# Performance work log

Hardware: AMD Instinct MI355X
Metric: run time of the kernel (lower is better)

## Reference

```python
import jax, jax.numpy as jnp
import numpy as np

N_NODES = 100000
N_EDGES = 3200000
NFEAT = 256
NHID = 256
NCLASS = 64


def setup_inputs() -> dict:
    key = jax.random.key(0)
    ks = jax.random.split(key, 12)
    x = jax.random.normal(ks[0], (N_NODES, NFEAT), dtype=jnp.float32)
    edge_src = jax.random.randint(ks[1], (N_EDGES,), 0, N_NODES, dtype=jnp.int32)
    edge_dst = jnp.sort(jax.random.randint(ks[2], (N_EDGES,), 0, N_NODES, dtype=jnp.int32))
    edge_w = jax.random.uniform(ks[3], (N_EDGES,), dtype=jnp.float32)
    s1 = 1.0 / np.sqrt(NFEAT)
    s2 = 1.0 / np.sqrt(NHID)
    W1 = jax.random.normal(ks[4], (NFEAT, NHID), dtype=jnp.float32) * s1
    b1 = jnp.zeros((NHID,), dtype=jnp.float32)
    W2 = jax.random.normal(ks[5], (NHID, NHID), dtype=jnp.float32) * s2
    b2 = jnp.zeros((NHID,), dtype=jnp.float32)
    WL1 = jax.random.normal(ks[6], (NHID, NCLASS), dtype=jnp.float32) * s2
    bL1 = jnp.zeros((NCLASS,), dtype=jnp.float32)
    WL2 = jax.random.normal(ks[7], (NHID, NCLASS), dtype=jnp.float32) * s2
    bL2 = jnp.zeros((NCLASS,), dtype=jnp.float32)
    return {"x": x, "edge_src": edge_src, "edge_dst": edge_dst, "edge_w": edge_w,
            "W1": W1, "b1": b1, "W2": W2, "b2": b2,
            "WL1": WL1, "bL1": bL1, "WL2": WL2, "bL2": bL2}


def reference(x, edge_src, edge_dst, edge_w, W1, b1, W2, b2, WL1, bL1, WL2, bL2):
    n = x.shape[0]

    def spmm(h):
        # adj @ h with adj given as (src, dst, w) edge list:
        # out[dst] += w * h[src]
        return jax.ops.segment_sum(edge_w[:, None] * h[edge_src], edge_dst, num_segments=n)

    # GraphConvolution layer 1: support = x @ W; out = adj @ support + b; relu
    # (dropout inactive in eval mode)
    h = jax.nn.relu(spmm(x @ W1) + b1)
    # GraphConvolution layer 2
    h = jax.nn.relu(spmm(h @ W2) + b2)
    # twin dense heads
    logit1 = h @ WL1 + bL1
    logit2 = h @ WL2 + bL2
    return (logit1, logit2)
```

## Files before the change

### kernel.cpp

```cpp
#include <hip/hip_runtime.h>
#include <hip/hip_bf16.h>

typedef __attribute__((ext_vector_type(8))) short short8;
typedef __attribute__((ext_vector_type(4))) float f32x4;
typedef __attribute__((ext_vector_type(2))) float f32x2;

__device__ inline unsigned short f2bf(float f) {
    union { float f; unsigned int u; } x; x.f = f;
    return (unsigned short)((x.u + 0x7fffu + ((x.u >> 16) & 1u)) >> 16);
}

#define ASYNC16(gptr, lptr)                                                      \
    __builtin_amdgcn_global_load_lds(                                            \
        (const __attribute__((address_space(1))) unsigned int*)(gptr),           \
        (__attribute__((address_space(3))) unsigned int*)(lptr), 16, 0, 0)

__device__ __host__ inline int sg(int j) {
    int p = j & 63;
    return (j & ~63) | ((p >> 2) + 16 * (p & 3));
}

__global__ void rowptr_kernel(const int* __restrict__ dst, int* __restrict__ rp,
                              int E, int N) {
    int e = blockIdx.x * blockDim.x + threadIdx.x;
    if (e >= E) return;
    int d1 = dst[e];
    int d0 = (e == 0) ? -1 : dst[e - 1];
    for (int n = d0 + 1; n <= d1; n++) rp[n] = e;
    if (e <= N) {
        int dlast = dst[E - 1];
        if (e > dlast) rp[e] = E;
    }
}

__global__ void x2bf_kernel(const float* __restrict__ x, unsigned short* __restrict__ xb,
                            int n8) {
    int i = blockIdx.x * blockDim.x + threadIdx.x;
    if (i >= n8) return;
    const uint4* p = (const uint4*)(x + (size_t)i * 8);
    uint4 u = p[0], v = p[1];
    uint4 pk;
    pk.x = ((u.x + 0x8000u) >> 16) | ((u.y + 0x8000u) & 0xffff0000u);
    pk.y = ((u.z + 0x8000u) >> 16) | ((u.w + 0x8000u) & 0xffff0000u);
    pk.z = ((v.x + 0x8000u) >> 16) | ((v.y + 0x8000u) & 0xffff0000u);
    pk.w = ((v.z + 0x8000u) >> 16) | ((v.w + 0x8000u) & 0xffff0000u);
    *(uint4*)(xb + (size_t)i * 8) = pk;
}

__global__ void prep_kernel(const float* __restrict__ W1, const float* __restrict__ W2,
                            const float* __restrict__ WL1, const float* __restrict__ WL2,
                            const float* __restrict__ b1, const float* __restrict__ b2,
                            unsigned short* __restrict__ W1t, unsigned short* __restrict__ W2t,
                            unsigned short* __restrict__ WLt,
                            float* __restrict__ b1p, float* __restrict__ b2p) {
    int b = blockIdx.x, k = threadIdx.x;
    if (b < 256) {
        W1t[(size_t)b * 256 + k] = f2bf(W1[(size_t)k * 256 + b]);
    } else if (b < 512) {
        int n = b - 256;
        W2t[(size_t)n * 256 + k] = f2bf(W2[(size_t)sg(k) * 256 + n]);
    } else if (b < 640) {
        int c = b - 512;
        int ks = sg(k);
        float v = (c < 64) ? WL1[(size_t)ks * 64 + c] : WL2[(size_t)ks * 64 + (c - 64)];
        WLt[(size_t)c * 256 + k] = f2bf(v);
    } else if (b == 640) {
        b1p[k] = b1[sg(k)];
    } else {
        b2p[k] = b2[sg(k)];
    }
}

__global__ __launch_bounds__(256) void gemm_f8_kernel(
    const unsigned short* __restrict__ A, const unsigned short* __restrict__ Bt,
    unsigned char* __restrict__ C, int M)
{
    __shared__ __align__(16) unsigned short As[128 * 32];
    __shared__ __align__(16) unsigned short Bs[128 * 32];
    const int t = threadIdx.x;
    const int row0 = blockIdx.y * 128;
    const int col0 = blockIdx.x * 128;
    const int wid = t >> 6, lane = t & 63;
    const int wm = (wid >> 1) * 64, wn = (wid & 1) * 64;
    const int qk = (lane >> 4) * 8, r16 = lane & 15;

    const int c0 = t, c1 = t + 256;
    const int am0 = min(row0 + (c0 >> 2), M - 1);
    const int am1 = min(row0 + (c1 >> 2), M - 1);
    const int ak0 = (c0 & 3) * 8, ak1 = (c1 & 3) * 8;
    const int bm0 = col0 + (c0 >> 2), bm1 = col0 + (c1 >> 2);

    f32x4 acc[4][4];
#pragma unroll
    for (int i = 0; i < 4; i++)
#pragma unroll
        for (int j = 0; j < 4; j++) acc[i][j] = (f32x4){0.f, 0.f, 0.f, 0.f};

    for (int k0 = 0; k0 < 256; k0 += 32) {
        ASYNC16(A + (size_t)am0 * 256 + k0 + ak0, &As[c0 * 8]);
        ASYNC16(A + (size_t)am1 * 256 + k0 + ak1, &As[c1 * 8]);
        ASYNC16(Bt + (size_t)bm0 * 256 + k0 + ak0, &Bs[c0 * 8]);
        ASYNC16(Bt + (size_t)bm1 * 256 + k0 + ak1, &Bs[c1 * 8]);
        __syncthreads();
        short8 av[4], bv[4];
#pragma unroll
        for (int mt = 0; mt < 4; mt++) av[mt] = *(const short8*)(&As[(wm + mt * 16 + r16) * 32 + qk]);
#pragma unroll
        for (int nt = 0; nt < 4; nt++) bv[nt] = *(const short8*)(&Bs[(wn + nt * 16 + r16) * 32 + qk]);
#pragma unroll
        for (int mt = 0; mt < 4; mt++)
#pragma unroll
            for (int nt = 0; nt < 4; nt++)
                acc[mt][nt] = __builtin_amdgcn_mfma_f32_16x16x32_bf16(av[mt], bv[nt], acc[mt][nt], 0, 0, 0);
        __syncthreads();
    }
#pragma unroll
    for (int mt = 0; mt < 4; mt++) {
        const int rowb = row0 + wm + mt * 16 + (lane >> 4) * 4;
#pragma unroll
        for (int r = 0; r < 4; r++) {
            const int row = rowb + r;
            if (row >= M) continue;
            int w = 0;
            w = __builtin_amdgcn_cvt_pk_fp8_f32(acc[mt][0][r], acc[mt][1][r], w, false);
            w = __builtin_amdgcn_cvt_pk_fp8_f32(acc[mt][2][r], acc[mt][3][r], w, true);
            *(unsigned int*)(C + (size_t)row * 256 + col0 + wn + r16 * 4) = (unsigned int)w;
        }
    }
}

__global__ __launch_bounds__(256) void head_kernel(
    const unsigned short* __restrict__ A, const unsigned short* __restrict__ Bt,
    const float* __restrict__ bL1, const float* __restrict__ bL2,
    float* __restrict__ out, int M)
{
    __shared__ __align__(16) unsigned short As[128 * 32];
    __shared__ __align__(16) unsigned short Bs[128 * 32];
    const int t = threadIdx.x;
    const int row0 = blockIdx.x * 128;
    const int wid = t >> 6, lane = t & 63;
    const int wm = (wid >> 1) * 64, wn = (wid & 1) * 64;
    const int qk = (lane >> 4) * 8, r16 = lane & 15;

    const int c0 = t, c1 = t + 256;
    const int am0 = min(row0 + (c0 >> 2), M - 1);
    const int am1 = min(row0 + (c1 >> 2), M - 1);
    const int ak0 = (c0 & 3) * 8, ak1 = (c1 & 3) * 8;
    const int bm0 = c0 >> 2, bm1 = c1 >> 2;

    f32x4 acc[4][4];
#pragma unroll
    for (int i = 0; i < 4; i++)
#pragma unroll
        for (int j = 0; j < 4; j++) acc[i][j] = (f32x4){0.f, 0.f, 0.f, 0.f};

    for (int k0 = 0; k0 < 256; k0 += 32) {
        ASYNC16(A + (size_t)am0 * 256 + k0 + ak0, &As[c0 * 8]);
        ASYNC16(A + (size_t)am1 * 256 + k0 + ak1, &As[c1 * 8]);
        ASYNC16(Bt + (size_t)bm0 * 256 + k0 + ak0, &Bs[c0 * 8]);
        ASYNC16(Bt + (size_t)bm1 * 256 + k0 + ak1, &Bs[c1 * 8]);
        __syncthreads();
        short8 av[4], bv[4];
#pragma unroll
        for (int mt = 0; mt < 4; mt++) av[mt] = *(const short8*)(&As[(wm + mt * 16 + r16) * 32 + qk]);
#pragma unroll
        for (int nt = 0; nt < 4; nt++) bv[nt] = *(const short8*)(&Bs[(wn + nt * 16 + r16) * 32 + qk]);
#pragma unroll
        for (int mt = 0; mt < 4; mt++)
#pragma unroll
            for (int nt = 0; nt < 4; nt++)
                acc[mt][nt] = __builtin_amdgcn_mfma_f32_16x16x32_bf16(av[mt], bv[nt], acc[mt][nt], 0, 0, 0);
        __syncthreads();
    }
#pragma unroll
    for (int mt = 0; mt < 4; mt++) {
#pragma unroll
        for (int r = 0; r < 4; r++) {
            int row = row0 + wm + mt * 16 + (lane >> 4) * 4 + r;
            if (row >= M) continue;
#pragma unroll
            for (int nt = 0; nt < 4; nt++) {
                int col = wn + nt * 16 + r16;
                float v = acc[mt][nt][r];
                if (col < 64) {
                    out[(size_t)row * 64 + col] = v + bL1[col];
                } else {
                    out[(size_t)M * 64 + (size_t)row * 64 + (col - 64)] = v + bL2[col - 64];
                }
            }
        }
    }
}

__device__ inline void acc16f8(float* a, uint4 r, float w) {
    f32x2 p;
    p = __builtin_amdgcn_cvt_pk_f32_fp8((int)r.x, false); a[0]  += w * p.x; a[1]  += w * p.y;
    p = __builtin_amdgcn_cvt_pk_f32_fp8((int)r.x, true);  a[2]  += w * p.x; a[3]  += w * p.y;
    p = __builtin_amdgcn_cvt_pk_f32_fp8((int)r.y, false); a[4]  += w * p.x; a[5]  += w * p.y;
    p = __builtin_amdgcn_cvt_pk_f32_fp8((int)r.y, true);  a[6]  += w * p.x; a[7]  += w * p.y;
    p = __builtin_amdgcn_cvt_pk_f32_fp8((int)r.z, false); a[8]  += w * p.x; a[9]  += w * p.y;
    p = __builtin_amdgcn_cvt_pk_f32_fp8((int)r.z, true);  a[10] += w * p.x; a[11] += w * p.y;
    p = __builtin_amdgcn_cvt_pk_f32_fp8((int)r.w, false); a[12] += w * p.x; a[13] += w * p.y;
    p = __builtin_amdgcn_cvt_pk_f32_fp8((int)r.w, true);  a[14] += w * p.x; a[15] += w * p.y;
}

__global__ __launch_bounds__(256) void spmm_fp8_kernel(
    const unsigned char* __restrict__ sup, const int* __restrict__ rp,
    const int* __restrict__ esrc, const float* __restrict__ ew,
    const float* __restrict__ bias, unsigned short* __restrict__ out, int nnodes)
{
    const int wid = threadIdx.x >> 6, lane = threadIdx.x & 63;
    const int node = blockIdx.x * 4 + wid;
    if (node >= nnodes) return;
    const int g = lane >> 4;
    const int f16 = (lane & 15) * 16;
    const unsigned char* supf = sup + f16;
    const int beg = rp[node], end = rp[node + 1];

    float a[16];
#pragma unroll
    for (int i = 0; i < 16; i++) a[i] = 0.f;

    int e = beg;
    for (; e + 8 <= end; e += 8) {
        const int s0 = esrc[e + g],     s1 = esrc[e + 4 + g];
        const float w0 = ew[e + g],     w1 = ew[e + 4 + g];
        const uint4 r0 = *(const uint4*)(supf + (size_t)s0 * 256);
        const uint4 r1 = *(const uint4*)(supf + (size_t)s1 * 256);
        acc16f8(a, r0, w0);
        acc16f8(a, r1, w1);
    }
    for (; e + 4 <= end; e += 4) {
        const int s = esrc[e + g];
        const float w = ew[e + g];
        const uint4 r = *(const uint4*)(supf + (size_t)s * 256);
        acc16f8(a, r, w);
    }
    {
        const int rem = end - e;
        if (g < rem) {
            const int s = esrc[e + g];
            const float w = ew[e + g];
            const uint4 r = *(const uint4*)(supf + (size_t)s * 256);
            acc16f8(a, r, w);
        }
    }
#pragma unroll
    for (int i = 0; i < 16; i++) {
        a[i] += __shfl_xor(a[i], 16);
        a[i] += __shfl_xor(a[i], 32);
    }

    if (g == 0) {
        const float4 b0 = *(const float4*)(bias + f16);
        const float4 b1 = *(const float4*)(bias + f16 + 4);
        const float4 b2 = *(const float4*)(bias + f16 + 8);
        const float4 b3 = *(const float4*)(bias + f16 + 12);
        a[0] += b0.x; a[1] += b0.y; a[2]  += b0.z; a[3]  += b0.w;
        a[4] += b1.x; a[5] += b1.y; a[6]  += b1.z; a[7]  += b1.w;
        a[8] += b2.x; a[9] += b2.y; a[10] += b2.z; a[11] += b2.w;
        a[12] += b3.x; a[13] += b3.y; a[14] += b3.z; a[15] += b3.w;
#pragma unroll
        for (int i = 0; i < 16; i++) a[i] = a[i] > 0.f ? a[i] : 0.f;
        uint4 o0, o1;
        o0.x = (unsigned int)f2bf(a[0])  | ((unsigned int)f2bf(a[1])  << 16);
        o0.y = (unsigned int)f2bf(a[2])  | ((unsigned int)f2bf(a[3])  << 16);
        o0.z = (unsigned int)f2bf(a[4])  | ((unsigned int)f2bf(a[5])  << 16);
        o0.w = (unsigned int)f2bf(a[6])  | ((unsigned int)f2bf(a[7])  << 16);
        o1.x = (unsigned int)f2bf(a[8])  | ((unsigned int)f2bf(a[9])  << 16);
        o1.y = (unsigned int)f2bf(a[10]) | ((unsigned int)f2bf(a[11]) << 16);
        o1.z = (unsigned int)f2bf(a[12]) | ((unsigned int)f2bf(a[13]) << 16);
        o1.w = (unsigned int)f2bf(a[14]) | ((unsigned int)f2bf(a[15]) << 16);
        *(uint4*)(out + (size_t)node * 256 + f16) = o0;
        *(uint4*)(out + (size_t)node * 256 + f16 + 8) = o1;
    }
}

extern "C" void kernel_launch(void* const* d_in, const int* in_sizes, int n_in,
                              void* d_out, int out_size, void* d_ws, size_t ws_size,
                              hipStream_t stream) {
    const float* x    = (const float*)d_in[0];
    const int*   esrc = (const int*)d_in[1];
    const int*   edst = (const int*)d_in[2];
    const float* ew   = (const float*)d_in[3];
    const float* W1   = (const float*)d_in[4];
    const float* b1   = (const float*)d_in[5];
    const float* W2   = (const float*)d_in[6];
    const float* b2   = (const float*)d_in[7];
    const float* WL1  = (const float*)d_in[8];
    const float* bL1  = (const float*)d_in[9];
    const float* WL2  = (const float*)d_in[10];
    const float* bL2  = (const float*)d_in[11];
    float* out = (float*)d_out;

    const int N = in_sizes[0] / 256;
    const int E = in_sizes[1];

    char* ws = (char*)d_ws;
    size_t off = 0;
    auto alloc = [&](size_t bytes) -> void* {
        void* p = ws + off;
        off = (off + bytes + 511) & ~(size_t)511;
        return p;
    };
    int* rp              = (int*)alloc((size_t)(N + 1) * 4);
    unsigned short* W1t  = (unsigned short*)alloc((size_t)256 * 256 * 2);
    unsigned short* W2t  = (unsigned short*)alloc((size_t)256 * 256 * 2);
    unsigned short* WLt  = (unsigned short*)alloc((size_t)128 * 256 * 2);
    float* b1p           = (float*)alloc(256 * 4);
    float* b2p           = (float*)alloc(256 * 4);
    unsigned char* sup8  = (unsigned char*)alloc((size_t)N * 256);
    unsigned short* hbuf = (unsigned short*)alloc((size_t)N * 256 * 2);

    const int mblocks = (N + 127) / 128;

    rowptr_kernel<<<(E + 255) / 256, 256, 0, stream>>>(edst, rp, E, N);
    x2bf_kernel<<<(N * 256 / 8 + 255) / 256, 256, 0, stream>>>(x, hbuf, N * 256 / 8);
    prep_kernel<<<642, 256, 0, stream>>>(W1, W2, WL1, WL2, b1, b2, W1t, W2t, WLt, b1p, b2p);

    gemm_f8_kernel<<<dim3(2, mblocks), 256, 0, stream>>>(hbuf, W1t, sup8, N);
    spmm_fp8_kernel<<<(N + 3) / 4, 256, 0, stream>>>(sup8, rp, esrc, ew, b1p, hbuf, N);
    gemm_f8_kernel<<<dim3(2, mblocks), 256, 0, stream>>>(hbuf, W2t, sup8, N);
    spmm_fp8_kernel<<<(N + 3) / 4, 256, 0, stream>>>(sup8, rp, esrc, ew, b2p, hbuf, N);
    head_kernel<<<mblocks, 256, 0, stream>>>(hbuf, WLt, bL1, bL2, out, N);
}
```

Measured before the change: 497.2 us.

## Slice fp8 support into 32-column planes and pack edge src/weight into one word

The GEMM now writes its fp8 output as eight column slices of 32 bytes per node. The SpMM is restructured so each block processes one slice for 64 nodes, with four lanes per node. Because each slice is only a fraction of the full support matrix, the random gathers should hit L2 and the MALL far more often. A new pre-pass packs each edge's source index and bf16-truncated weight into one 32-bit word, halving edge-stream traffic (read once per slice), and the edge loads use nontemporal hints. In exchange, the edge list is re-read eight times per layer and edge weights lose precision to bf16.

```diff
diff --git a/kernel.cpp b/kernel.cpp
--- a/kernel.cpp
+++ b/kernel.cpp
@@ -6,6 +6,11 @@
 typedef __attribute__((ext_vector_type(2))) float f32x2;
 
 __device__ inline unsigned short f2bf(float f) {
+    union { float f; unsigned int u; } x; x.f = f;
+    return (unsigned short)((x.u + 0x7fffu + ((x.u >> 16) & 1u)) >> 16);
+}
+
+__host__ inline unsigned short f2bf_h(float f) {
     union { float f; unsigned int u; } x; x.f = f;
     return (unsigned short)((x.u + 0x7fffu + ((x.u >> 16) & 1u)) >> 16);
 }
@@ -31,6 +36,24 @@
         int dlast = dst[E - 1];
         if (e > dlast) rp[e] = E;
     }
+}
+
+__global__ void epack_kernel(const int* __restrict__ src, const float* __restrict__ w,
+                             unsigned int* __restrict__ ep, int E4) {
+    int i = blockIdx.x * blockDim.x + threadIdx.x;
+    if (i >= E4) return;
+    const int4 sv = ((const int4*)src)[i];
+    const float4 wv = ((const float4*)w)[i];
+    uint4 o;
+    o.x = ((unsigned int)(f2bf(wv.x) & 0x7fffu) << 17) | (unsigned int)sv.x;
+    o.y = ((unsigned int)(f2bf(wv.y) & 0x7fffu) << 17) | (unsigned int)sv.y;
+    o.z = ((unsigned int)(f2bf(wv.z) & 0x7fffu) << 17) | (unsigned int)sv.z;
+    o.w = ((unsigned int)(f2bf(wv.w) & 0x7fffu) << 17) | (unsigned int)sv.w;
+    ((uint4*)ep)[i] = o;
+}
+
+__device__ inline float unpackw(unsigned int p) {
+    return __uint_as_float((p >> 17) << 16);
 }
 
 __global__ void x2bf_kernel(const float* __restrict__ x, unsigned short* __restrict__ xb,
@@ -114,6 +137,8 @@
                 acc[mt][nt] = __builtin_amdgcn_mfma_f32_16x16x32_bf16(av[mt], bv[nt], acc[mt][nt], 0, 0, 0);
         __syncthreads();
     }
+    const int scol = col0 + wn + r16 * 4;
+    unsigned char* cb = C + (size_t)(scol >> 5) * ((size_t)M * 32) + (scol & 31);
 #pragma unroll
     for (int mt = 0; mt < 4; mt++) {
         const int rowb = row0 + wm + mt * 16 + (lane >> 4) * 4;
@@ -124,7 +149,7 @@
             int w = 0;
             w = __builtin_amdgcn_cvt_pk_fp8_f32(acc[mt][0][r], acc[mt][1][r], w, false);
             w = __builtin_amdgcn_cvt_pk_fp8_f32(acc[mt][2][r], acc[mt][3][r], w, true);
-            *(unsigned int*)(C + (size_t)row * 256 + col0 + wn + r16 * 4) = (unsigned int)w;
+            *(unsigned int*)(cb + (size_t)row * 32) = (unsigned int)w;
         }
     }
 }
@@ -204,58 +229,72 @@
     p = __builtin_amdgcn_cvt_pk_f32_fp8((int)r.w, true);  a[14] += w * p.x; a[15] += w * p.y;
 }
 
-__global__ __launch_bounds__(256) void spmm_fp8_kernel(
+template <bool PACKED>
+__global__ __launch_bounds__(256) void spmm_slice_kernel(
     const unsigned char* __restrict__ sup, const int* __restrict__ rp,
-    const int* __restrict__ esrc, const float* __restrict__ ew,
-    const float* __restrict__ bias, unsigned short* __restrict__ out, int nnodes)
+    const unsigned int* __restrict__ ep, const int* __restrict__ esrc,
+    const float* __restrict__ ew, const float* __restrict__ bias,
+    unsigned short* __restrict__ out, int nnodes)
 {
-    const int wid = threadIdx.x >> 6, lane = threadIdx.x & 63;
-    const int node = blockIdx.x * 4 + wid;
-    if (node >= nnodes) return;
-    const int g = lane >> 4;
-    const int f16 = (lane & 15) * 16;
-    const unsigned char* supf = sup + f16;
-    const int beg = rp[node], end = rp[node + 1];
+    const int s    = blockIdx.x & 7;
+    const int nb   = blockIdx.x >> 3;
+    const int lane = threadIdx.x & 63;
+    const int wid  = threadIdx.x >> 6;
+    const int node = nb * 64 + wid * 16 + (lane >> 2);
+    const int slot = (lane >> 1) & 1;
+    const int h    = lane & 1;
+    const int nc   = node < nnodes ? node : nnodes - 1;
+    const int beg  = rp[nc], end = rp[nc + 1];
+    const unsigned char* sups = sup + (size_t)s * ((size_t)nnodes * 32) + h * 16;
 
     float a[16];
 #pragma unroll
     for (int i = 0; i < 16; i++) a[i] = 0.f;
 
-    int e = beg;
-    for (; e + 8 <= end; e += 8) {
-        const int s0 = esrc[e + g],     s1 = esrc[e + 4 + g];
-        const float w0 = ew[e + g],     w1 = ew[e + 4 + g];
-        const uint4 r0 = *(const uint4*)(supf + (size_t)s0 * 256);
-        const uint4 r1 = *(const uint4*)(supf + (size_t)s1 * 256);
+    int e = beg + slot;
+    for (; e + 2 < end; e += 4) {
+        int s0i, s1i; float w0, w1;
+        if (PACKED) {
+            const unsigned int p0 = __builtin_nontemporal_load(ep + e);
+            const unsigned int p1 = __builtin_nontemporal_load(ep + e + 2);
+            s0i = (int)(p0 & 0x1ffffu);
+            s1i = (int)(p1 & 0x1ffffu);
+            w0 = unpackw(p0);
+            w1 = unpackw(p1);
+        } else {
+            s0i = __builtin_nontemporal_load(esrc + e);
+            s1i = __builtin_nontemporal_load(esrc + e + 2);
+            w0  = __builtin_nontemporal_load(ew + e);
+            w1  = __builtin_nontemporal_load(ew + e + 2);
+        }
+        const uint4 r0 = *(const uint4*)(sups + (size_t)s0i * 32);
+        const uint4 r1 = *(const uint4*)(sups + (size_t)s1i * 32);
         acc16f8(a, r0, w0);
         acc16f8(a, r1, w1);
     }
-    for (; e + 4 <= end; e += 4) {
-        const int s = esrc[e + g];
-        const float w = ew[e + g];
-        const uint4 r = *(const uint4*)(supf + (size_t)s * 256);
+    if (e < end) {
+        int si; float w;
+        if (PACKED) {
+            const unsigned int p = __builtin_nontemporal_load(ep + e);
+            si = (int)(p & 0x1ffffu);
+            w = unpackw(p);
+        } else {
+            si = __builtin_nontemporal_load(esrc + e);
+            w  = __builtin_nontemporal_load(ew + e);
+        }
+        const uint4 r = *(const uint4*)(sups + (size_t)si * 32);
         acc16f8(a, r, w);
     }
-    {
-        const int rem = end - e;
-        if (g < rem) {
-            const int s = esrc[e + g];
-            const float w = ew[e + g];
-            const uint4 r = *(const uint4*)(supf + (size_t)s * 256);
-            acc16f8(a, r, w);
-        }
-    }
-#pragma unroll
-    for (int i = 0; i < 16; i++) {
-        a[i] += __shfl_xor(a[i], 16);
-        a[i] += __shfl_xor(a[i], 32);
-    }
-
-    if (g == 0) {
-        const float4 b0 = *(const float4*)(bias + f16);
-        const float4 b1 = *(const float4*)(bias + f16 + 4);
-        const float4 b2 = *(const float4*)(bias + f16 + 8);
-        const float4 b3 = *(const float4*)(bias + f16 + 12);
+
+#pragma unroll
+    for (int i = 0; i < 16; i++) a[i] += __shfl_xor(a[i], 2);
+
+    if (slot == 0 && node < nnodes) {
+        const int fb = s * 32 + h * 16;
+        const float4 b0 = *(const float4*)(bias + fb);
+        const float4 b1 = *(const float4*)(bias + fb + 4);
+        const float4 b2 = *(const float4*)(bias + fb + 8);
+        const float4 b3 = *(const float4*)(bias + fb + 12);
         a[0] += b0.x; a[1] += b0.y; a[2]  += b0.z; a[3]  += b0.w;
         a[4] += b1.x; a[5] += b1.y; a[6]  += b1.z; a[7]  += b1.w;
         a[8] += b2.x; a[9] += b2.y; a[10] += b2.z; a[11] += b2.w;
@@ -271,8 +310,9 @@
         o1.y = (unsigned int)f2bf(a[10]) | ((unsigned int)f2bf(a[11]) << 16);
         o1.z = (unsigned int)f2bf(a[12]) | ((unsigned int)f2bf(a[13]) << 16);
         o1.w = (unsigned int)f2bf(a[14]) | ((unsigned int)f2bf(a[15]) << 16);
-        *(uint4*)(out + (size_t)node * 256 + f16) = o0;
-        *(uint4*)(out + (size_t)node * 256 + f16 + 8) = o1;
+        unsigned short* op = out + (size_t)node * 256 + fb;
+        *(uint4*)op = o0;
+        *(uint4*)(op + 8) = o1;
     }
 }
 
@@ -311,16 +351,27 @@
     float* b2p           = (float*)alloc(256 * 4);
     unsigned char* sup8  = (unsigned char*)alloc((size_t)N * 256);
     unsigned short* hbuf = (unsigned short*)alloc((size_t)N * 256 * 2);
+    unsigned int* ep     = (unsigned int*)alloc((size_t)E * 4);
+    const bool packed = (off <= ws_size);
 
     const int mblocks = (N + 127) / 128;
+    const int sblocks = 8 * ((N + 63) / 64);
 
     rowptr_kernel<<<(E + 255) / 256, 256, 0, stream>>>(edst, rp, E, N);
+    if (packed)
+        epack_kernel<<<(E / 4 + 255) / 256, 256, 0, stream>>>(esrc, ew, ep, E / 4);
     x2bf_kernel<<<(N * 256 / 8 + 255) / 256, 256, 0, stream>>>(x, hbuf, N * 256 / 8);
     prep_kernel<<<642, 256, 0, stream>>>(W1, W2, WL1, WL2, b1, b2, W1t, W2t, WLt, b1p, b2p);
 
     gemm_f8_kernel<<<dim3(2, mblocks), 256, 0, stream>>>(hbuf, W1t, sup8, N);
-    spmm_fp8_kernel<<<(N + 3) / 4, 256, 0, stream>>>(sup8, rp, esrc, ew, b1p, hbuf, N);
+    if (packed)
+        spmm_slice_kernel<true><<<sblocks, 256, 0, stream>>>(sup8, rp, ep, esrc, ew, b1p, hbuf, N);
+    else
+        spmm_slice_kernel<false><<<sblocks, 256, 0, stream>>>(sup8, rp, ep, esrc, ew, b1p, hbuf, N);
     gemm_f8_kernel<<<dim3(2, mblocks), 256, 0, stream>>>(hbuf, W2t, sup8, N);
-    spmm_fp8_kernel<<<(N + 3) / 4, 256, 0, stream>>>(sup8, rp, esrc, ew, b2p, hbuf, N);
+    if (packed)
+        spmm_slice_kernel<true><<<sblocks, 256, 0, stream>>>(sup8, rp, ep, esrc, ew, b2p, hbuf, N);
+    else
+        spmm_slice_kernel<false><<<sblocks, 256, 0, stream>>>(sup8, rp, ep, esrc, ew, b2p, hbuf, N);
     head_kernel<<<mblocks, 256, 0, stream>>>(hbuf, WLt, bL1, bL2, out, N);
 }
```

Result: slower. 929.8 us (+87.0%).

## Pack edge source and bf16 weight into one word with software-pipelined gathers

Applied to the files above, without the earlier changes.

A new pre-pass packs each edge's 17-bit source index and a truncated 15-bit bf16 weight into a single 32-bit word. Both SpMM passes then read this one array instead of two separate index and weight arrays. The new SpMM also prefetches edge words two groups ahead and feature rows one group ahead, to hide gather latency. The weight loses precision (bf16, sign bit dropped), and the pack pass costs an extra read and write of the edge list. The packing assumes fewer than 131072 nodes and non-negative weights.

```diff
diff --git a/kernel.cpp b/kernel.cpp
--- a/kernel.cpp
+++ b/kernel.cpp
@@ -31,6 +31,24 @@
         int dlast = dst[E - 1];
         if (e > dlast) rp[e] = E;
     }
+}
+
+__global__ void epack_kernel(const int* __restrict__ src, const float* __restrict__ w,
+                             unsigned int* __restrict__ ep, int E4) {
+    int i = blockIdx.x * blockDim.x + threadIdx.x;
+    if (i >= E4) return;
+    const int4 sv = ((const int4*)src)[i];
+    const float4 wv = ((const float4*)w)[i];
+    uint4 o;
+    o.x = ((unsigned int)(f2bf(wv.x) & 0x7fffu) << 17) | (unsigned int)sv.x;
+    o.y = ((unsigned int)(f2bf(wv.y) & 0x7fffu) << 17) | (unsigned int)sv.y;
+    o.z = ((unsigned int)(f2bf(wv.z) & 0x7fffu) << 17) | (unsigned int)sv.z;
+    o.w = ((unsigned int)(f2bf(wv.w) & 0x7fffu) << 17) | (unsigned int)sv.w;
+    ((uint4*)ep)[i] = o;
+}
+
+__device__ inline float unpackw(unsigned int p) {
+    return __uint_as_float((p >> 17) << 16);
 }
 
 __global__ void x2bf_kernel(const float* __restrict__ x, unsigned short* __restrict__ xb,
@@ -206,6 +224,94 @@
 
 __global__ __launch_bounds__(256) void spmm_fp8_kernel(
     const unsigned char* __restrict__ sup, const int* __restrict__ rp,
+    const unsigned int* __restrict__ ep, const float* __restrict__ bias,
+    unsigned short* __restrict__ out, int nnodes)
+{
+    const int wid = threadIdx.x >> 6, lane = threadIdx.x & 63;
+    const int node = blockIdx.x * 4 + wid;
+    if (node >= nnodes) return;
+    const int g = lane >> 4;
+    const int f16 = (lane & 15) * 16;
+    const unsigned char* supf = sup + f16;
+    const int beg = rp[node], end = rp[node + 1];
+
+    float a[16];
+#pragma unroll
+    for (int i = 0; i < 16; i++) a[i] = 0.f;
+
+    int e = beg;
+    const int nmain = (end - beg) >> 3;
+    if (nmain > 0) {
+        unsigned int cp0 = ep[e + g], cp1 = ep[e + 4 + g];
+        uint4 cr0 = *(const uint4*)(supf + (size_t)(cp0 & 0x1ffffu) * 256);
+        uint4 cr1 = *(const uint4*)(supf + (size_t)(cp1 & 0x1ffffu) * 256);
+        unsigned int np0 = 0, np1 = 0;
+        if (nmain > 1) {
+            np0 = ep[e + 8 + g]; np1 = ep[e + 12 + g];
+        }
+        for (int it = 0; it + 1 < nmain; ++it) {
+            const uint4 nr0 = *(const uint4*)(supf + (size_t)(np0 & 0x1ffffu) * 256);
+            const uint4 nr1 = *(const uint4*)(supf + (size_t)(np1 & 0x1ffffu) * 256);
+            unsigned int mp0 = 0, mp1 = 0;
+            if (it + 2 < nmain) {
+                const int eb = e + (it + 2) * 8;
+                mp0 = ep[eb + g]; mp1 = ep[eb + 4 + g];
+            }
+            acc16f8(a, cr0, unpackw(cp0));
+            acc16f8(a, cr1, unpackw(cp1));
+            cr0 = nr0; cr1 = nr1; cp0 = np0; cp1 = np1;
+            np0 = mp0; np1 = mp1;
+        }
+        acc16f8(a, cr0, unpackw(cp0));
+        acc16f8(a, cr1, unpackw(cp1));
+        e += nmain * 8;
+    }
+    for (; e + 4 <= end; e += 4) {
+        const unsigned int p = ep[e + g];
+        const uint4 r = *(const uint4*)(supf + (size_t)(p & 0x1ffffu) * 256);
+        acc16f8(a, r, unpackw(p));
+    }
+    {
+        const int rem = end - e;
+        if (g < rem) {
+            const unsigned int p = ep[e + g];
+            const uint4 r = *(const uint4*)(supf + (size_t)(p & 0x1ffffu) * 256);
+            acc16f8(a, r, unpackw(p));
+        }
+    }
+#pragma unroll
+    for (int i = 0; i < 16; i++) {
+        a[i] += __shfl_xor(a[i], 16);
+        a[i] += __shfl_xor(a[i], 32);
+    }
+
+    if (g == 0) {
+        const float4 b0 = *(const float4*)(bias + f16);
+        const float4 b1 = *(const float4*)(bias + f16 + 4);
+        const float4 b2 = *(const float4*)(bias + f16 + 8);
+        const float4 b3 = *(const float4*)(bias + f16 + 12);
+        a[0] += b0.x; a[1] += b0.y; a[2]  += b0.z; a[3]  += b0.w;
+        a[4] += b1.x; a[5] += b1.y; a[6]  += b1.z; a[7]  += b1.w;
+        a[8] += b2.x; a[9] += b2.y; a[10] += b2.z; a[11] += b2.w;
+        a[12] += b3.x; a[13] += b3.y; a[14] += b3.z; a[15] += b3.w;
+#pragma unroll
+        for (int i = 0; i < 16; i++) a[i] = a[i] > 0.f ? a[i] : 0.f;
+        uint4 o0, o1;
+        o0.x = (unsigned int)f2bf(a[0])  | ((unsigned int)f2bf(a[1])  << 16);
+        o0.y = (unsigned int)f2bf(a[2])  | ((unsigned int)f2bf(a[3])  << 16);
+        o0.z = (unsigned int)f2bf(a[4])  | ((unsigned int)f2bf(a[5])  << 16);
+        o0.w = (unsigned int)f2bf(a[6])  | ((unsigned int)f2bf(a[7])  << 16);
+        o1.x = (unsigned int)f2bf(a[8])  | ((unsigned int)f2bf(a[9])  << 16);
+        o1.y = (unsigned int)f2bf(a[10]) | ((unsigned int)f2bf(a[11]) << 16);
+        o1.z = (unsigned int)f2bf(a[12]) | ((unsigned int)f2bf(a[13]) << 16);
+        o1.w = (unsigned int)f2bf(a[14]) | ((unsigned int)f2bf(a[15]) << 16);
+        *(uint4*)(out + (size_t)node * 256 + f16) = o0;
+        *(uint4*)(out + (size_t)node * 256 + f16 + 8) = o1;
+    }
+}
+
+__global__ __launch_bounds__(256) void spmm_fp8_raw_kernel(
+    const unsigned char* __restrict__ sup, const int* __restrict__ rp,
     const int* __restrict__ esrc, const float* __restrict__ ew,
     const float* __restrict__ bias, unsigned short* __restrict__ out, int nnodes)
 {
@@ -311,16 +417,26 @@
     float* b2p           = (float*)alloc(256 * 4);
     unsigned char* sup8  = (unsigned char*)alloc((size_t)N * 256);
     unsigned short* hbuf = (unsigned short*)alloc((size_t)N * 256 * 2);
+    unsigned int* ep     = (unsigned int*)alloc((size_t)E * 4);
+    const bool packed = (off <= ws_size);
 
     const int mblocks = (N + 127) / 128;
 
     rowptr_kernel<<<(E + 255) / 256, 256, 0, stream>>>(edst, rp, E, N);
+    if (packed)
+        epack_kernel<<<(E / 4 + 255) / 256, 256, 0, stream>>>(esrc, ew, ep, E / 4);
     x2bf_kernel<<<(N * 256 / 8 + 255) / 256, 256, 0, stream>>>(x, hbuf, N * 256 / 8);
     prep_kernel<<<642, 256, 0, stream>>>(W1, W2, WL1, WL2, b1, b2, W1t, W2t, WLt, b1p, b2p);
 
     gemm_f8_kernel<<<dim3(2, mblocks), 256, 0, stream>>>(hbuf, W1t, sup8, N);
-    spmm_fp8_kernel<<<(N + 3) / 4, 256, 0, stream>>>(sup8, rp, esrc, ew, b1p, hbuf, N);
+    if (packed)
+        spmm_fp8_kernel<<<(N + 3) / 4, 256, 0, stream>>>(sup8, rp, ep, b1p, hbuf, N);
+    else
+        spmm_fp8_raw_kernel<<<(N + 3) / 4, 256, 0, stream>>>(sup8, rp, esrc, ew, b1p, hbuf, N);
     gemm_f8_kernel<<<dim3(2, mblocks), 256, 0, stream>>>(hbuf, W2t, sup8, N);
-    spmm_fp8_kernel<<<(N + 3) / 4, 256, 0, stream>>>(sup8, rp, esrc, ew, b2p, hbuf, N);
+    if (packed)
+        spmm_fp8_kernel<<<(N + 3) / 4, 256, 0, stream>>>(sup8, rp, ep, b2p, hbuf, N);
+    else
+        spmm_fp8_raw_kernel<<<(N + 3) / 4, 256, 0, stream>>>(sup8, rp, esrc, ew, b2p, hbuf, N);
     head_kernel<<<mblocks, 256, 0, stream>>>(hbuf, WLt, bL1, bL2, out, N);
 }
```

New measurement: 506.2 us. About the same (+1.8%).
